# Kernel optimization log

Measured on AMD Instinct MI355X. Metric: run time of the kernel, lower is better.

The kernel has to match this reference:

```python
import jax, jax.numpy as jnp
import numpy as np

B, C, H, W = 16, 512, 96, 48
SE_C = C // 16  # se bottleneck = 32
BN_EPS = 1e-5


def setup_inputs() -> dict:
    key = jax.random.key(0)
    ks = jax.random.split(key, 16)
    s = 0.02
    return {
        "x": jax.random.normal(ks[0], (B, C, H, W), jnp.float32),
        # SE gate: C -> SE_C -> C (1x1 convs stored as dense matrices)
        "se_w1": jax.random.normal(ks[1], (SE_C, C), jnp.float32) * s,
        "se_b1": jnp.zeros((SE_C,), jnp.float32),
        "se_w2": jax.random.normal(ks[2], (C, SE_C), jnp.float32) * s,
        "se_b2": jnp.zeros((C,), jnp.float32),
        # g / theta / phi: 1x1 convs C -> 1 (weight is a C-vector, scalar bias)
        "g_w": jax.random.normal(ks[3], (C,), jnp.float32) * s,
        "g_b": jnp.zeros((), jnp.float32),
        "theta_w": jax.random.normal(ks[4], (C,), jnp.float32) * s,
        "theta_b": jnp.zeros((), jnp.float32),
        "phi_w": jax.random.normal(ks[5], (C,), jnp.float32) * s,
        "phi_b": jnp.zeros((), jnp.float32),
        # W: 1x1 conv 1 -> C, followed by BatchNorm2d(C) (inference stats).
        # NOTE: torch inits BN gamma/beta to 0 (output would be exactly x);
        # we use random gamma/beta so the whole graph contributes to output/grads.
        "W_w": jax.random.normal(ks[6], (C,), jnp.float32) * s,
        "W_b": jnp.zeros((C,), jnp.float32),
        "bn_gamma": jax.random.normal(ks[7], (C,), jnp.float32) * 0.1 + 1.0,
        "bn_beta": jax.random.normal(ks[8], (C,), jnp.float32) * 0.1,
        "bn_mean": jax.random.normal(ks[9], (C,), jnp.float32) * 0.1,
        "bn_var": jax.random.uniform(ks[10], (C,), jnp.float32, 0.5, 1.5),
    }


def reference(x, se_w1, se_b1, se_w2, se_b2, g_w, g_b, theta_w, theta_b,
              phi_w, phi_b, W_w, W_b, bn_gamma, bn_beta, bn_mean, bn_var):
    b, c, h, w = x.shape
    n = h * w
    # SE channel gate on global-avg-pooled features
    xp = x.mean(axis=(2, 3))                                  # (b, c)
    hid = jax.nn.relu(xp @ se_w1.T + se_b1)                   # (b, se_c)
    gate = jax.nn.sigmoid(hid @ se_w2.T + se_b2)              # (b, c)
    xc = gate[:, :, None, None] * x                           # (b, c, h, w)
    # 1x1 C->1 projections, flattened over spatial positions
    g_x = jnp.einsum('bchw,c->bhw', xc, g_w).reshape(b, n) + g_b       # (b, n)
    th = jnp.einsum('bchw,c->bhw', xc, theta_w).reshape(b, n) + theta_b
    ph = jnp.einsum('bchw,c->bhw', xc, phi_w).reshape(b, n) + phi_b
    # f = theta phi^T / N; y = f g. inter_channels==1 => rank-1, contract phi.g first
    s = jnp.sum(ph * g_x, axis=-1, keepdims=True) / n          # (b, 1)
    y = (th * s).reshape(b, 1, h, w)                           # (b, 1, h, w)
    # W: 1x1 conv 1->C then BatchNorm2d (inference form)
    wy = y * W_w[None, :, None, None] + W_b[None, :, None, None]
    inv = bn_gamma / jnp.sqrt(bn_var + BN_EPS)
    wy = (wy - bn_mean[None, :, None, None]) * inv[None, :, None, None] \
         + bn_beta[None, :, None, None]
    return wy + x
```

## Files before the change

### kernel.cpp

```cpp
#include <hip/hip_runtime.h>
#include <math.h>

#define BB   16
#define CCH  512
#define HWN  4608
#define HW4  1152
#define HW2  2304
#define NSE  32
#define BN_EPS 1e-5f

#define NCH  8
#define CPC  64

typedef float f32x4 __attribute__((ext_vector_type(4)));

__global__ __launch_bounds__(256) void k_mean(const float* __restrict__ x,
                                              float* __restrict__ xp) {
    int wave = threadIdx.x >> 6;
    int lane = threadIdx.x & 63;
    int row = blockIdx.x * 4 + wave;
    const float4* xr = (const float4*)x + (size_t)row * HW4;
    float s = 0.f;
    #pragma unroll
    for (int k = 0; k < 18; ++k) {
        float4 v = xr[lane + k * 64];
        s += v.x + v.y + v.z + v.w;
    }
    #pragma unroll
    for (int off = 32; off > 0; off >>= 1)
        s += __shfl_down(s, off);
    if (lane == 0) xp[row] = s * (1.0f / (float)HWN);
}

__global__ __launch_bounds__(512) void k_gate(
    const float* __restrict__ xp,
    const float* __restrict__ se_w1, const float* __restrict__ se_b1,
    const float* __restrict__ se_w2, const float* __restrict__ se_b2,
    const float* __restrict__ g_w, const float* __restrict__ theta_w,
    const float* __restrict__ phi_w,
    float* __restrict__ tw, float* __restrict__ pw, float* __restrict__ gw,
    float* __restrict__ sacc) {
    __shared__ float xs[CCH];
    __shared__ float hs[NSE];
    int b = blockIdx.x, t = threadIdx.x;
    int wave = t >> 6, lane = t & 63;
    if (t == 0) sacc[b] = 0.f;
    xs[t] = xp[b * CCH + t];
    __syncthreads();
    #pragma unroll
    for (int i = 0; i < 4; ++i) {
        int h = wave * 4 + i;
        const float* wr = se_w1 + h * CCH;
        float a = 0.f;
        #pragma unroll
        for (int k = 0; k < 8; ++k)
            a += wr[lane + 64 * k] * xs[lane + 64 * k];
        #pragma unroll
        for (int off = 32; off > 0; off >>= 1)
            a += __shfl_down(a, off);
        if (lane == 0) {
            a += se_b1[h];
            hs[h] = a > 0.f ? a : 0.f;
        }
    }
    __syncthreads();
    float a = se_b2[t];
    const float* wr = se_w2 + t * NSE;
    #pragma unroll
    for (int j = 0; j < NSE; ++j) a += wr[j] * hs[j];
    float gate = 1.f / (1.f + expf(-a));
    int idx = b * CCH + t;
    tw[idx] = gate * theta_w[t];
    pw[idx] = gate * phi_w[t];
    gw[idx] = gate * g_w[t];
}

__global__ __launch_bounds__(128) void k_proj(
    const float* __restrict__ x,
    const float* __restrict__ tw, const float* __restrict__ pw,
    const float* __restrict__ gw,
    float* __restrict__ th_part, float* __restrict__ ph_part,
    float* __restrict__ gx_part) {
    __shared__ float tws[CPC], pws[CPC], gws[CPC];
    int t = threadIdx.x;
    int b = blockIdx.z;
    int ch = blockIdx.y;
    int c0 = ch * CPC;
    int p4 = blockIdx.x * 128 + t;
    if (t < CPC) {
        int wi = b * CCH + c0 + t;
        tws[t] = tw[wi]; pws[t] = pw[wi]; gws[t] = gw[wi];
    }
    __syncthreads();
    const float4* xr = (const float4*)x + (size_t)(b * CCH + c0) * HW4 + p4;
    float4 tha = {0.f, 0.f, 0.f, 0.f};
    float4 pha = {0.f, 0.f, 0.f, 0.f};
    float4 gxa = {0.f, 0.f, 0.f, 0.f};
    #pragma unroll 8
    for (int c = 0; c < CPC; ++c) {
        float4 v = xr[(size_t)c * HW4];
        float tc = tws[c], pc = pws[c], gc = gws[c];
        tha.x += tc * v.x; tha.y += tc * v.y; tha.z += tc * v.z; tha.w += tc * v.w;
        pha.x += pc * v.x; pha.y += pc * v.y; pha.z += pc * v.z; pha.w += pc * v.w;
        gxa.x += gc * v.x; gxa.y += gc * v.y; gxa.z += gc * v.z; gxa.w += gc * v.w;
    }
    size_t oi = (size_t)(ch * BB + b) * HW4 + p4;
    ((float4*)th_part)[oi] = tha;
    ((float4*)ph_part)[oi] = pha;
    ((float4*)gx_part)[oi] = gxa;
}

__global__ __launch_bounds__(128) void k_sred(
    const float* __restrict__ ph_part, const float* __restrict__ gx_part,
    const float* __restrict__ phi_b, const float* __restrict__ g_b,
    float* __restrict__ sacc) {
    int t = threadIdx.x;
    int b = blockIdx.y;
    int i = blockIdx.x * 128 + t;
    float pb = phi_b[0], gb = g_b[0];
    const float4* php = (const float4*)ph_part;
    const float4* gxp = (const float4*)gx_part;
    float4 ph = {pb, pb, pb, pb};
    float4 gx = {gb, gb, gb, gb};
    #pragma unroll
    for (int k = 0; k < NCH; ++k) {
        size_t oi = (size_t)(k * BB + b) * HW4 + i;
        float4 pv = php[oi];
        float4 gv = gxp[oi];
        ph.x += pv.x; ph.y += pv.y; ph.z += pv.z; ph.w += pv.w;
        gx.x += gv.x; gx.y += gv.y; gx.z += gv.z; gx.w += gv.w;
    }
    float acc = ph.x * gx.x + ph.y * gx.y + ph.z * gx.z + ph.w * gx.w;
    #pragma unroll
    for (int off = 32; off > 0; off >>= 1)
        acc += __shfl_down(acc, off);
    __shared__ float ws0;
    if (t == 64) ws0 = acc;
    __syncthreads();
    if (t == 0) atomicAdd(&sacc[b], acc + ws0);
}

__global__ __launch_bounds__(128) void k_ths(
    const float* __restrict__ th_part, const float* __restrict__ theta_b,
    const float* __restrict__ sacc, float* __restrict__ ths) {
    int t = threadIdx.x;
    int b = blockIdx.y;
    int i = blockIdx.x * 128 + t;
    float s = sacc[b] * (1.0f / (float)HWN);
    float tb = theta_b[0];
    const float4* thp = (const float4*)th_part;
    float4 th = {tb, tb, tb, tb};
    #pragma unroll
    for (int k = 0; k < NCH; ++k) {
        float4 tv = thp[(size_t)(k * BB + b) * HW4 + i];
        th.x += tv.x; th.y += tv.y; th.z += tv.z; th.w += tv.w;
    }
    float4 o = {th.x * s, th.y * s, th.z * s, th.w * s};
    ((float4*)ths)[(size_t)b * HW4 + i] = o;
}

__global__ __launch_bounds__(256) void k_out(
    const float* __restrict__ x, const float* __restrict__ ths,
    const float* __restrict__ W_w, const float* __restrict__ W_b,
    const float* __restrict__ bn_gamma, const float* __restrict__ bn_beta,
    const float* __restrict__ bn_mean, const float* __restrict__ bn_var,
    float* __restrict__ out) {
    int wave = threadIdx.x >> 6;
    int lane = threadIdx.x & 63;
    int c = blockIdx.x * 4 + wave;
    int b = blockIdx.y;
    float inv = bn_gamma[c] * rsqrtf(bn_var[c] + BN_EPS);
    float A = W_w[c] * inv;
    float Dc = (W_b[c] - bn_mean[c]) * inv + bn_beta[c];
    const float4* xr = (const float4*)x + (size_t)(b * CCH + c) * HW4;
    const float4* tr = (const float4*)ths + (size_t)b * HW4;
    f32x4* orow = (f32x4*)out + (size_t)(b * CCH + c) * HW4;
    #pragma unroll
    for (int k = 0; k < 18; ++k) {
        int i = lane + k * 64;
        float4 xv = xr[i];
        float4 tv = tr[i];
        f32x4 o;
        o.x = xv.x + tv.x * A + Dc;
        o.y = xv.y + tv.y * A + Dc;
        o.z = xv.z + tv.z * A + Dc;
        o.w = xv.w + tv.w * A + Dc;
        __builtin_nontemporal_store(o, &orow[i]);
    }
}

extern "C" void kernel_launch(void* const* d_in, const int* in_sizes, int n_in,
                              void* d_out, int out_size, void* d_ws, size_t ws_size,
                              hipStream_t stream) {
    const float* x       = (const float*)d_in[0];
    const float* se_w1   = (const float*)d_in[1];
    const float* se_b1   = (const float*)d_in[2];
    const float* se_w2   = (const float*)d_in[3];
    const float* se_b2   = (const float*)d_in[4];
    const float* g_w     = (const float*)d_in[5];
    const float* g_b     = (const float*)d_in[6];
    const float* theta_w = (const float*)d_in[7];
    const float* theta_b = (const float*)d_in[8];
    const float* phi_w   = (const float*)d_in[9];
    const float* phi_b   = (const float*)d_in[10];
    const float* W_w     = (const float*)d_in[11];
    const float* W_b     = (const float*)d_in[12];
    const float* bn_g    = (const float*)d_in[13];
    const float* bn_b    = (const float*)d_in[14];
    const float* bn_m    = (const float*)d_in[15];
    const float* bn_v    = (const float*)d_in[16];
    float* out = (float*)d_out;

    float* ws      = (float*)d_ws;
    float* xp      = ws;
    float* tw      = ws + 8192;
    float* pw      = ws + 16384;
    float* gwv     = ws + 24576;
    float* th_part = ws + 32768;
    float* ph_part = ws + 32768 + 589824;
    float* gx_part = ws + 32768 + 2 * 589824;
    float* ths     = ws + 32768 + 3 * 589824;
    float* sacc    = ws + 32768 + 3 * 589824 + 73728;

    k_mean<<<BB * CCH / 4, 256, 0, stream>>>(x, xp);
    k_gate<<<BB, CCH, 0, stream>>>(xp, se_w1, se_b1, se_w2, se_b2,
                                   g_w, theta_w, phi_w, tw, pw, gwv, sacc);
    dim3 gc(9, NCH, BB);
    k_proj<<<gc, 128, 0, stream>>>(x, tw, pw, gwv, th_part, ph_part, gx_part);
    dim3 gs(9, BB);
    k_sred<<<gs, 128, 0, stream>>>(ph_part, gx_part, phi_b, g_b, sacc);
    k_ths<<<gs, 128, 0, stream>>>(th_part, theta_b, sacc, ths);
    dim3 gd(CCH / 4, BB);
    k_out<<<gd, 256, 0, stream>>>(x, ths, W_w, W_b, bn_g, bn_b, bn_m, bn_v, out);
}
```

Baseline: 339.9 us.

## Fuse mean+gate and proj+reduce kernels via last-block atomic counters

Merges the channel-mean kernel with the SE gate computation by having the last block per batch (detected via an atomic counter) compute the gate. Likewise folds the phi·g reduction and theta scaling into the projection kernel, with the last block per batch doing the serial reduction. This removes three kernel launches and the inter-kernel gaps, adding a memset. In exchange, the final per-batch work runs in a single 128-thread block, which serialises the partial-sum reduction and may lengthen the tail.

```diff
diff --git a/kernel.cpp b/kernel.cpp
--- a/kernel.cpp
+++ b/kernel.cpp
@@ -5,7 +5,6 @@
 #define CCH  512
 #define HWN  4608
 #define HW4  1152
-#define HW2  2304
 #define NSE  32
 #define BN_EPS 1e-5f
 
@@ -14,42 +13,47 @@
 
 typedef float f32x4 __attribute__((ext_vector_type(4)));
 
-__global__ __launch_bounds__(256) void k_mean(const float* __restrict__ x,
-                                              float* __restrict__ xp) {
-    int wave = threadIdx.x >> 6;
-    int lane = threadIdx.x & 63;
-    int row = blockIdx.x * 4 + wave;
-    const float4* xr = (const float4*)x + (size_t)row * HW4;
-    float s = 0.f;
-    #pragma unroll
-    for (int k = 0; k < 18; ++k) {
-        float4 v = xr[lane + k * 64];
-        s += v.x + v.y + v.z + v.w;
-    }
-    #pragma unroll
-    for (int off = 32; off > 0; off >>= 1)
-        s += __shfl_down(s, off);
-    if (lane == 0) xp[row] = s * (1.0f / (float)HWN);
-}
-
-__global__ __launch_bounds__(512) void k_gate(
-    const float* __restrict__ xp,
+__global__ __launch_bounds__(256) void k_mean_gate(
+    const float* __restrict__ x,
     const float* __restrict__ se_w1, const float* __restrict__ se_b1,
     const float* __restrict__ se_w2, const float* __restrict__ se_b2,
     const float* __restrict__ g_w, const float* __restrict__ theta_w,
     const float* __restrict__ phi_w,
-    float* __restrict__ tw, float* __restrict__ pw, float* __restrict__ gw,
-    float* __restrict__ sacc) {
+    float* __restrict__ xp, float* __restrict__ tw, float* __restrict__ pw,
+    float* __restrict__ gw, unsigned int* __restrict__ cnt)
+{
     __shared__ float xs[CCH];
     __shared__ float hs[NSE];
-    int b = blockIdx.x, t = threadIdx.x;
+    __shared__ unsigned int lastflag;
+    int t = threadIdx.x;
     int wave = t >> 6, lane = t & 63;
-    if (t == 0) sacc[b] = 0.f;
-    xs[t] = xp[b * CCH + t];
-    __syncthreads();
-    #pragma unroll
-    for (int i = 0; i < 4; ++i) {
-        int h = wave * 4 + i;
+    int row = blockIdx.x * 4 + wave;
+    int b = row >> 9;
+    const float4* xr = (const float4*)x + (size_t)row * HW4;
+    float s = 0.f;
+    #pragma unroll
+    for (int k = 0; k < 18; ++k) {
+        float4 v = xr[lane + k * 64];
+        s += v.x + v.y + v.z + v.w;
+    }
+    #pragma unroll
+    for (int off = 32; off > 0; off >>= 1)
+        s += __shfl_down(s, off);
+    if (lane == 0) xp[row] = s * (1.0f / (float)HWN);
+
+    __threadfence();
+    __syncthreads();
+    if (t == 0) lastflag = (atomicAdd(&cnt[b], 1u) == 127u) ? 1u : 0u;
+    __syncthreads();
+    if (!lastflag) return;
+    __threadfence();
+
+    xs[t]       = xp[b * CCH + t];
+    xs[t + 256] = xp[b * CCH + 256 + t];
+    __syncthreads();
+    #pragma unroll
+    for (int i = 0; i < 8; ++i) {
+        int h = wave * 8 + i;
         const float* wr = se_w1 + h * CCH;
         float a = 0.f;
         #pragma unroll
@@ -64,24 +68,35 @@
         }
     }
     __syncthreads();
-    float a = se_b2[t];
-    const float* wr = se_w2 + t * NSE;
-    #pragma unroll
-    for (int j = 0; j < NSE; ++j) a += wr[j] * hs[j];
-    float gate = 1.f / (1.f + expf(-a));
-    int idx = b * CCH + t;
-    tw[idx] = gate * theta_w[t];
-    pw[idx] = gate * phi_w[t];
-    gw[idx] = gate * g_w[t];
-}
-
-__global__ __launch_bounds__(128) void k_proj(
+    #pragma unroll
+    for (int cc = 0; cc < 2; ++cc) {
+        int c = t + cc * 256;
+        float a = se_b2[c];
+        const float* wr = se_w2 + c * NSE;
+        #pragma unroll
+        for (int j = 0; j < NSE; ++j) a += wr[j] * hs[j];
+        float gate = 1.f / (1.f + expf(-a));
+        int idx = b * CCH + c;
+        tw[idx] = gate * theta_w[c];
+        pw[idx] = gate * phi_w[c];
+        gw[idx] = gate * g_w[c];
+    }
+}
+
+__global__ __launch_bounds__(128) void k_proj_s(
     const float* __restrict__ x,
     const float* __restrict__ tw, const float* __restrict__ pw,
     const float* __restrict__ gw,
+    const float* __restrict__ theta_b, const float* __restrict__ phi_b,
+    const float* __restrict__ g_b,
     float* __restrict__ th_part, float* __restrict__ ph_part,
-    float* __restrict__ gx_part) {
+    float* __restrict__ gx_part, float* __restrict__ ths,
+    unsigned int* __restrict__ cnt)
+{
     __shared__ float tws[CPC], pws[CPC], gws[CPC];
+    __shared__ float red[2];
+    __shared__ float s_sh;
+    __shared__ unsigned int lastflag;
     int t = threadIdx.x;
     int b = blockIdx.z;
     int ch = blockIdx.y;
@@ -108,55 +123,51 @@
     ((float4*)th_part)[oi] = tha;
     ((float4*)ph_part)[oi] = pha;
     ((float4*)gx_part)[oi] = gxa;
-}
-
-__global__ __launch_bounds__(128) void k_sred(
-    const float* __restrict__ ph_part, const float* __restrict__ gx_part,
-    const float* __restrict__ phi_b, const float* __restrict__ g_b,
-    float* __restrict__ sacc) {
-    int t = threadIdx.x;
-    int b = blockIdx.y;
-    int i = blockIdx.x * 128 + t;
+
+    __threadfence();
+    __syncthreads();
+    if (t == 0) lastflag = (atomicAdd(&cnt[b], 1u) == 71u) ? 1u : 0u;
+    __syncthreads();
+    if (!lastflag) return;
+    __threadfence();
+
     float pb = phi_b[0], gb = g_b[0];
     const float4* php = (const float4*)ph_part;
     const float4* gxp = (const float4*)gx_part;
-    float4 ph = {pb, pb, pb, pb};
-    float4 gx = {gb, gb, gb, gb};
-    #pragma unroll
-    for (int k = 0; k < NCH; ++k) {
-        size_t oi = (size_t)(k * BB + b) * HW4 + i;
-        float4 pv = php[oi];
-        float4 gv = gxp[oi];
-        ph.x += pv.x; ph.y += pv.y; ph.z += pv.z; ph.w += pv.w;
-        gx.x += gv.x; gx.y += gv.y; gx.z += gv.z; gx.w += gv.w;
-    }
-    float acc = ph.x * gx.x + ph.y * gx.y + ph.z * gx.z + ph.w * gx.w;
+    float acc = 0.f;
+    for (int i = t; i < HW4; i += 128) {
+        float4 ph = {pb, pb, pb, pb};
+        float4 gx = {gb, gb, gb, gb};
+        #pragma unroll
+        for (int k = 0; k < NCH; ++k) {
+            size_t q = (size_t)(k * BB + b) * HW4 + i;
+            float4 pv = php[q];
+            float4 gv = gxp[q];
+            ph.x += pv.x; ph.y += pv.y; ph.z += pv.z; ph.w += pv.w;
+            gx.x += gv.x; gx.y += gv.y; gx.z += gv.z; gx.w += gv.w;
+        }
+        acc += ph.x * gx.x + ph.y * gx.y + ph.z * gx.z + ph.w * gx.w;
+    }
     #pragma unroll
     for (int off = 32; off > 0; off >>= 1)
         acc += __shfl_down(acc, off);
-    __shared__ float ws0;
-    if (t == 64) ws0 = acc;
-    __syncthreads();
-    if (t == 0) atomicAdd(&sacc[b], acc + ws0);
-}
-
-__global__ __launch_bounds__(128) void k_ths(
-    const float* __restrict__ th_part, const float* __restrict__ theta_b,
-    const float* __restrict__ sacc, float* __restrict__ ths) {
-    int t = threadIdx.x;
-    int b = blockIdx.y;
-    int i = blockIdx.x * 128 + t;
-    float s = sacc[b] * (1.0f / (float)HWN);
+    if ((t & 63) == 0) red[t >> 6] = acc;
+    __syncthreads();
+    if (t == 0) s_sh = (red[0] + red[1]) * (1.0f / (float)HWN);
+    __syncthreads();
+    float s = s_sh;
     float tb = theta_b[0];
     const float4* thp = (const float4*)th_part;
-    float4 th = {tb, tb, tb, tb};
-    #pragma unroll
-    for (int k = 0; k < NCH; ++k) {
-        float4 tv = thp[(size_t)(k * BB + b) * HW4 + i];
-        th.x += tv.x; th.y += tv.y; th.z += tv.z; th.w += tv.w;
-    }
-    float4 o = {th.x * s, th.y * s, th.z * s, th.w * s};
-    ((float4*)ths)[(size_t)b * HW4 + i] = o;
+    for (int i = t; i < HW4; i += 128) {
+        float4 th = {tb, tb, tb, tb};
+        #pragma unroll
+        for (int k = 0; k < NCH; ++k) {
+            float4 tv = thp[(size_t)(k * BB + b) * HW4 + i];
+            th.x += tv.x; th.y += tv.y; th.z += tv.z; th.w += tv.w;
+        }
+        float4 o = {th.x * s, th.y * s, th.z * s, th.w * s};
+        ((float4*)ths)[(size_t)b * HW4 + i] = o;
+    }
 }
 
 __global__ __launch_bounds__(256) void k_out(
@@ -220,16 +231,17 @@
     float* ph_part = ws + 32768 + 589824;
     float* gx_part = ws + 32768 + 2 * 589824;
     float* ths     = ws + 32768 + 3 * 589824;
-    float* sacc    = ws + 32768 + 3 * 589824 + 73728;
-
-    k_mean<<<BB * CCH / 4, 256, 0, stream>>>(x, xp);
-    k_gate<<<BB, CCH, 0, stream>>>(xp, se_w1, se_b1, se_w2, se_b2,
-                                   g_w, theta_w, phi_w, tw, pw, gwv, sacc);
+    unsigned int* cnt = (unsigned int*)(ths + 73728);
+
+    hipMemsetAsync(cnt, 0, 32 * sizeof(unsigned int), stream);
+
+    k_mean_gate<<<BB * CCH / 4, 256, 0, stream>>>(
+        x, se_w1, se_b1, se_w2, se_b2, g_w, theta_w, phi_w,
+        xp, tw, pw, gwv, cnt);
     dim3 gc(9, NCH, BB);
-    k_proj<<<gc, 128, 0, stream>>>(x, tw, pw, gwv, th_part, ph_part, gx_part);
-    dim3 gs(9, BB);
-    k_sred<<<gs, 128, 0, stream>>>(ph_part, gx_part, phi_b, g_b, sacc);
-    k_ths<<<gs, 128, 0, stream>>>(th_part, theta_b, sacc, ths);
+    k_proj_s<<<gc, 128, 0, stream>>>(
+        x, tw, pw, gwv, theta_b, phi_b, g_b,
+        th_part, ph_part, gx_part, ths, cnt + BB);
     dim3 gd(CCH / 4, BB);
     k_out<<<gd, 256, 0, stream>>>(x, ths, W_w, W_b, bn_g, bn_b, bn_m, bn_v, out);
 }
```

After: 782.1 us. +130.1%, slower.
